# Performance work log

Hardware: AMD Instinct MI355X
Metric: run time of the kernel (lower is better)

Reference implementation:

```python
import jax, jax.numpy as jnp
import numpy as np

L = 2000          # number of residues (sequence length)
FEATURES_L = 2048 # config.features_L pad target
W = 7             # config.window_size
D = 54            # per-residue feature dim after bert_lin
H = 3             # attention heads
HD = D // H       # head dim = 18
CH = 32           # conv hidden channels
KS = (3, 5, 7)    # config.kernels


def setup_inputs() -> dict:
    key = jax.random.key(0)
    ks = jax.random.split(key, 20)
    n = lambda k, s, sc=0.02: jax.random.normal(k, s, jnp.float32) * sc
    return {
        'beft_f': jax.random.normal(ks[0], (L, 1024), jnp.float32),
        'pssm_f': jax.random.normal(ks[1], (L, 20), jnp.float32),
        'hmm_f': jax.random.normal(ks[2], (L, 30), jnp.float32),
        'dssp_f': jax.random.normal(ks[3], (L, 14), jnp.float32),
        'W_bert': n(ks[4], (1024, D)), 'b_bert': jnp.zeros((D,), jnp.float32),
        'ln_g1': jnp.ones((D,), jnp.float32), 'ln_b1': jnp.zeros((D,), jnp.float32),
        'ln_g2': jnp.ones((D,), jnp.float32), 'ln_b2': jnp.zeros((D,), jnp.float32),
        'conv1_w': n(ks[5], (CH, 1, 3, 1), 0.1), 'conv1_b': n(ks[6], (CH,), 0.1),
        'prelu_a': jnp.array(0.25, jnp.float32),
        'conv2_w': n(ks[7], (CH, 1, 5, 1), 0.1), 'conv2_b': n(ks[8], (CH,), 0.1),
        'conv3_w': n(ks[9], (CH, 1, 7, 1), 0.1), 'conv3_b': n(ks[10], (CH,), 0.1),
        'W1': n(ks[11], (972, 256)), 'b1': jnp.zeros((256,), jnp.float32),
        'W2': n(ks[12], (CH * 256, 256)), 'b2': jnp.zeros((256,), jnp.float32),
    }


def _ln(x, g, b, eps=1e-5):
    m = x.mean(-1, keepdims=True)
    v = ((x - m) ** 2).mean(-1, keepdims=True)
    return (x - m) * jax.lax.rsqrt(v + eps) * g + b


def _attn(x, g, b):
    # x: (L, W, D); no qkv projections, no 1/sqrt(d) scaling (as in source)
    qh = x.reshape(x.shape[0], W, H, HD)
    s = jnp.einsum('bqhd,bkhd->bhqk', qh, qh)
    p = jax.nn.softmax(s, axis=-1)
    o = jnp.einsum('bhqk,bkhd->bqhd', p, qh).reshape(x.shape[0], W, D)
    return _ln(o, g, b)


def _conv_branch(x, w, bias, k, act):
    pad = (k - 1) // 2
    c = jax.lax.conv_general_dilated(x, w, (1, 1), ((pad, pad), (0, 0)),
                                     dimension_numbers=('NCHW', 'OIHW', 'NCHW'))
    c = act(c + bias[None, :, None, None])
    c = jax.lax.reduce_window(c, -jnp.inf, jax.lax.max,
                              (1, 1, k, 1), (1, 1, 1, 1), 'VALID')
    return c.reshape(c.shape[0], CH, -1)  # (FEATURES_L, 32, (W-k+1)*2D)


def _forward(beft_f, W_bert, b_bert, ln_g1, ln_b1, ln_g2, ln_b2,
             conv1_w, conv1_b, prelu_a, conv2_w, conv2_b, conv3_w, conv3_b,
             W1, b1, W2, b2):
    f = beft_f @ W_bert + b_bert  # (L, 54)
    # sliding-window gather replicating the source python loop exactly:
    # interior rows i in (W, L-W): window = f[i-4 : i+3]; boundary rows: [f[i], 0...0]
    i = jnp.arange(L)
    j = jnp.arange(W)
    gidx = jnp.clip(i[:, None] - (W // 2 + 1) + j[None, :], 0, L - 1)
    win_int = f[gidx]                                   # (L, 7, 54)
    win_bnd = jnp.zeros((L, W, D), f.dtype).at[:, 0].set(f)
    boundary = (i <= W) | (i + W >= L)
    new_f = jnp.where(boundary[:, None, None], win_bnd, win_int)
    sf = _attn(new_f, ln_g1, ln_b1)
    sf = _attn(sf, ln_g2, ln_b2)
    cat = jnp.concatenate([new_f, sf], axis=2)          # (L, 7, 108)
    x = jnp.pad(cat, ((0, FEATURES_L - L), (0, 0), (0, 0)))[:, None]  # (FL,1,7,108)
    prelu = lambda z: jnp.where(z >= 0, z, prelu_a * z)
    feats = jnp.concatenate([
        _conv_branch(x, conv1_w, conv1_b, KS[0], prelu),
        _conv_branch(x, conv2_w, conv2_b, KS[1], jax.nn.relu),
        _conv_branch(x, conv3_w, conv3_b, KS[2], jax.nn.relu)], axis=2)  # (FL,32,972)
    y = feats[:L] @ W1 + b1                             # (L, 32, 256)
    y = y.reshape(L, CH * 256) @ W2 + b2                # (L, 256)
    return jnp.where(y >= 0, y, 0.01 * y)               # leaky_relu


def reference(beft_f, pssm_f, hmm_f, dssp_f, W_bert, b_bert, ln_g1, ln_b1,
              ln_g2, ln_b2, conv1_w, conv1_b, prelu_a, conv2_w, conv2_b,
              conv3_w, conv3_b, W1, b1, W2, b2):
    # pssm_f / hmm_f / dssp_f are accepted but unused in the source forward
    return _forward(beft_f, W_bert, b_bert, ln_g1, ln_b1, ln_g2, ln_b2,
                    conv1_w, conv1_b, prelu_a, conv2_w, conv2_b,
                    conv3_w, conv3_b, W1, b1, W2, b2)
```

## Files before the change

kernel.cpp:

```cpp
#include <hip/hip_runtime.h>

#define L_RES 2000
#define DF 54
#define WIN 7

typedef short bf16x8 __attribute__((ext_vector_type(8)));
typedef float f32x4 __attribute__((ext_vector_type(4)));
typedef unsigned short ushort8v __attribute__((ext_vector_type(8)));

__device__ __forceinline__ unsigned short f2bf(float f) {
    unsigned int u = __float_as_uint(f);
    unsigned int r = (u + 0x7FFFu + ((u >> 16) & 1u)) >> 16;
    return (unsigned short)r;
}
__device__ __forceinline__ float bf2f(unsigned short h) {
    return __uint_as_float(((unsigned int)h) << 16);
}
__device__ __forceinline__ void gload16(const unsigned short* g, unsigned short* l) {
    __builtin_amdgcn_global_load_lds(
        (const __attribute__((address_space(1))) void*)g,
        (__attribute__((address_space(3))) void*)l, 16, 0, 0);
}

__global__ __launch_bounds__(256) void split_beft(const float* __restrict__ beft,
                                                  unsigned short* __restrict__ A2) {
    int l = blockIdx.x;
    int t = threadIdx.x;
    unsigned short* row = A2 + (size_t)l * 3072;
    for (int k = t; k < 1024; k += 256) {
        unsigned short hi = 0, lo = 0;
        if (l < L_RES) {
            float x = beft[(size_t)l * 1024 + k];
            hi = f2bf(x);
            lo = f2bf(x - bf2f(hi));
        }
        row[k] = hi;
        row[1024 + k] = lo;
        row[2048 + k] = hi;
    }
}

__global__ __launch_bounds__(256) void b2t_build(const float* __restrict__ Wb,
                                                 unsigned short* __restrict__ B2T) {
    int idx = blockIdx.x * 256 + threadIdx.x;
    int n = idx / 3072, col = idx % 3072;
    int seg = col >> 10, k = col & 1023;
    unsigned short r = 0;
    if (n < DF) {
        float v = Wb[(size_t)k * DF + n];
        unsigned short hi = f2bf(v);
        r = (seg < 2) ? hi : f2bf(v - bf2f(hi));
    }
    B2T[idx] = r;
}

__global__ __launch_bounds__(256) void bert_mfma(const unsigned short* __restrict__ A2,
                                                 const unsigned short* __restrict__ B2T,
                                                 float* __restrict__ bpart) {
    __shared__ unsigned short ldsA[128 * 64];
    __shared__ unsigned short ldsB[64 * 64];
    int t = threadIdx.x, w = t >> 6, lane = t & 63;
    int m0 = blockIdx.x * 128;
    int z = blockIdx.y;
    long koff = (long)z * 768;
    int wr = w >> 1, wc = w & 1;
    int arow = lane & 15, kgrp = lane >> 4;

    const unsigned short* aS[4]; const unsigned short* bS[2];
    int aD[4], bD[2];
    #pragma unroll
    for (int j = 0; j < 4; ++j) {
        int s = j * 256 + t, r = s >> 3, c = s & 7;
        aS[j] = A2 + koff + (size_t)(m0 + r) * 3072 + c * 8;
        aD[j] = r * 64 + ((c ^ (r & 7)) * 8);
    }
    #pragma unroll
    for (int j = 0; j < 2; ++j) {
        int s = j * 256 + t, r = s >> 3, c = s & 7;
        bS[j] = B2T + koff + (size_t)r * 3072 + c * 8;
        bD[j] = r * 64 + ((c ^ (r & 7)) * 8);
    }
    f32x4 acc[4][2];
    #pragma unroll
    for (int mi = 0; mi < 4; ++mi)
        #pragma unroll
        for (int ni = 0; ni < 2; ++ni) acc[mi][ni] = (f32x4)(0.f);

    ushort8v va[4], vb[2];
    #pragma unroll
    for (int j = 0; j < 4; ++j) va[j] = *(const ushort8v*)(aS[j]);
    #pragma unroll
    for (int j = 0; j < 2; ++j) vb[j] = *(const ushort8v*)(bS[j]);

    for (int ks = 0; ks < 12; ++ks) {
        __syncthreads();
        #pragma unroll
        for (int j = 0; j < 4; ++j) *(ushort8v*)&ldsA[aD[j]] = va[j];
        #pragma unroll
        for (int j = 0; j < 2; ++j) *(ushort8v*)&ldsB[bD[j]] = vb[j];
        __syncthreads();
        if (ks + 1 < 12) {
            #pragma unroll
            for (int j = 0; j < 4; ++j) va[j] = *(const ushort8v*)(aS[j] + (ks + 1) * 64);
            #pragma unroll
            for (int j = 0; j < 2; ++j) vb[j] = *(const ushort8v*)(bS[j] + (ks + 1) * 64);
        }
        #pragma unroll
        for (int kk = 0; kk < 2; ++kk) {
            int chunk = kk * 4 + kgrp;
            bf16x8 af[4], bfr[2];
            #pragma unroll
            for (int mi = 0; mi < 4; ++mi) {
                int rl = wr * 64 + mi * 16 + arow;
                af[mi] = *(const bf16x8*)&ldsA[rl * 64 + ((chunk ^ (rl & 7)) * 8)];
            }
            #pragma unroll
            for (int ni = 0; ni < 2; ++ni) {
                int rl = wc * 32 + ni * 16 + arow;
                bfr[ni] = *(const bf16x8*)&ldsB[rl * 64 + ((chunk ^ (rl & 7)) * 8)];
            }
            #pragma unroll
            for (int mi = 0; mi < 4; ++mi)
                #pragma unroll
                for (int ni = 0; ni < 2; ++ni)
                    acc[mi][ni] = __builtin_amdgcn_mfma_f32_16x16x32_bf16(af[mi], bfr[ni], acc[mi][ni], 0, 0, 0);
        }
    }
    #pragma unroll
    for (int ni = 0; ni < 2; ++ni) {
        int n = wc * 32 + ni * 16 + arow;
        #pragma unroll
        for (int mi = 0; mi < 4; ++mi)
            #pragma unroll
            for (int r = 0; r < 4; ++r) {
                int m = m0 + wr * 64 + mi * 16 + kgrp * 4 + r;
                bpart[((size_t)z * 2048 + m) * 64 + n] = acc[mi][ni][r];
            }
    }
}

__global__ __launch_bounds__(64) void bert_reduce(const float* __restrict__ bpart,
                                                  const float* __restrict__ bb,
                                                  float* __restrict__ f) {
    int l = blockIdx.x, n = threadIdx.x;
    if (n < DF) {
        float s = bb[n];
        #pragma unroll
        for (int z = 0; z < 4; ++z) s += bpart[((size_t)z * 2048 + l) * 64 + n];
        f[(size_t)l * DF + n] = s;
    }
}

__device__ __forceinline__ void attn_layer(const float (*in)[DF], float (*out)[DF],
                                           float (*s)[WIN][WIN],
                                           const float* __restrict__ g,
                                           const float* __restrict__ b,
                                           float* mm, float* vv, int t) {
    for (int idx = t; idx < 3 * WIN * WIN; idx += 64) {
        int h = idx / 49, r = idx % 49, q = r / WIN, k = r % WIN;
        float sum = 0.f;
        #pragma unroll
        for (int d = 0; d < 18; ++d) sum = fmaf(in[q][h * 18 + d], in[k][h * 18 + d], sum);
        s[h][q][k] = sum;
    }
    __syncthreads();
    for (int idx = t; idx < 3 * WIN; idx += 64) {
        int h = idx / WIN, q = idx % WIN;
        float mx = s[h][q][0];
        #pragma unroll
        for (int k = 1; k < WIN; ++k) mx = fmaxf(mx, s[h][q][k]);
        float e[WIN], sum = 0.f;
        #pragma unroll
        for (int k = 0; k < WIN; ++k) { e[k] = expf(s[h][q][k] - mx); sum += e[k]; }
        float inv = 1.f / sum;
        #pragma unroll
        for (int k = 0; k < WIN; ++k) s[h][q][k] = e[k] * inv;
    }
    __syncthreads();
    for (int idx = t; idx < WIN * DF; idx += 64) {
        int q = idx / DF, c = idx % DF, h = c / 18;
        float sum = 0.f;
        #pragma unroll
        for (int k = 0; k < WIN; ++k) sum = fmaf(s[h][q][k], in[k][c], sum);
        out[q][c] = sum;
    }
    __syncthreads();
    for (int q = t; q < WIN; q += 64) {
        float m = 0.f;
        for (int c = 0; c < DF; ++c) m += out[q][c];
        m *= (1.f / DF);
        float v = 0.f;
        for (int c = 0; c < DF; ++c) { float d0 = out[q][c] - m; v = fmaf(d0, d0, v); }
        v *= (1.f / DF);
        mm[q] = m; vv[q] = rsqrtf(v + 1e-5f);
    }
    __syncthreads();
    for (int idx = t; idx < WIN * DF; idx += 64) {
        int q = idx / DF, c = idx % DF;
        out[q][c] = (out[q][c] - mm[q]) * vv[q] * g[c] + b[c];
    }
    __syncthreads();
}

__global__ __launch_bounds__(64) void window_attn(const float* __restrict__ f,
                                                  const float* __restrict__ g1,
                                                  const float* __restrict__ b1,
                                                  const float* __restrict__ g2,
                                                  const float* __restrict__ b2,
                                                  float* __restrict__ cat) {
    int l = blockIdx.x;
    int t = threadIdx.x;
    __shared__ float w[WIN][DF], o1[WIN][DF], o2[WIN][DF];
    __shared__ float s[3][WIN][WIN];
    __shared__ float mm[WIN], vv[WIN];
    bool boundary = (l <= WIN) || (l + WIN >= L_RES);
    for (int idx = t; idx < WIN * DF; idx += 64) {
        int j = idx / DF, d = idx % DF;
        w[j][d] = boundary ? (j == 0 ? f[(size_t)l * DF + d] : 0.f)
                           : f[(size_t)(l - 4 + j) * DF + d];
    }
    __syncthreads();
    attn_layer(w, o1, s, g1, b1, mm, vv, t);
    attn_layer(o1, o2, s, g2, b2, mm, vv, t);
    for (int idx = t; idx < WIN * DF; idx += 64) {
        int j = idx / DF, d = idx % DF;
        cat[(size_t)l * 756 + j * 108 + d] = w[j][d];
        cat[(size_t)l * 756 + j * 108 + DF + d] = o2[j][d];
    }
}

__global__ __launch_bounds__(256) void transpose_to_bf16(const float* __restrict__ src,
                                                         unsigned short* __restrict__ dst,
                                                         int M, int N, int Mpad) {
    __shared__ float tile[32][33];
    int m0 = blockIdx.x * 32, n0 = blockIdx.y * 32;
    int c = threadIdx.x % 32, r0 = threadIdx.x / 32;
    #pragma unroll
    for (int rr = 0; rr < 4; ++rr) {
        int r = r0 + rr * 8, m = m0 + r;
        tile[r][c] = (m < M) ? src[(size_t)m * N + n0 + c] : 0.f;
    }
    __syncthreads();
    #pragma unroll
    for (int rr = 0; rr < 4; ++rr) {
        int r = r0 + rr * 8;
        dst[(size_t)(n0 + r) * Mpad + m0 + c] = f2bf(tile[c][r]);
    }
}

__global__ __launch_bounds__(256) void conv_pool(
        const float* __restrict__ cat,
        const float* __restrict__ c1w, const float* __restrict__ c1b,
        const float* __restrict__ pa_p,
        const float* __restrict__ c2w, const float* __restrict__ c2b,
        const float* __restrict__ c3w, const float* __restrict__ c3b,
        unsigned short* __restrict__ Ap, int lbase) {
    int bid = blockIdx.x;
    int b = bid >> 2;
    int ch0 = (bid & 3) * 8;
    int l0 = lbase + b * 4;
    int t = threadIdx.x;
    __shared__ float catl[4 * 756];
    for (int i = t; i < 3024; i += 256) catl[i] = cat[(size_t)l0 * 756 + i];
    __syncthreads();
    float pa = pa_p[0];
    unsigned short* base = Ap + (size_t)b * 128 * 1024;
    int res = t >> 6, dp = t & 63;
    if (dp < 54) {
        int d0 = dp * 2;
        const float* cr = catl + res * 756;
        float colA[WIN], colB[WIN];
        #pragma unroll
        for (int h = 0; h < WIN; ++h) {
            colA[h] = cr[h * 108 + d0];
            colB[h] = cr[h * 108 + d0 + 1];
        }
        for (int c = ch0; c < ch0 + 8; ++c) {
            unsigned short* Arow = base + (size_t)(res * 32 + c) * 1024;
            {
                float w0 = c1w[c * 3], w1 = c1w[c * 3 + 1], w2 = c1w[c * 3 + 2];
                float bb = c1b[c];
                float vA[WIN], vB[WIN];
                #pragma unroll
                for (int h = 0; h < WIN; ++h) {
                    float sA = bb, sB = bb;
                    if (h >= 1) { sA = fmaf(w0, colA[h - 1], sA); sB = fmaf(w0, colB[h - 1], sB); }
                    sA = fmaf(w1, colA[h], sA); sB = fmaf(w1, colB[h], sB);
                    if (h <= 5) { sA = fmaf(w2, colA[h + 1], sA); sB = fmaf(w2, colB[h + 1], sB); }
                    vA[h] = sA >= 0.f ? sA : pa * sA;
                    vB[h] = sB >= 0.f ? sB : pa * sB;
                }
                #pragma unroll
                for (int p = 0; p < 5; ++p) {
                    unsigned int ua = f2bf(fmaxf(fmaxf(vA[p], vA[p + 1]), vA[p + 2]));
                    unsigned int ub = f2bf(fmaxf(fmaxf(vB[p], vB[p + 1]), vB[p + 2]));
                    *(unsigned int*)&Arow[p * 108 + d0] = ua | (ub << 16);
                }
            }
            {
                float wg[5], bb = c2b[c];
                #pragma unroll
                for (int x = 0; x < 5; ++x) wg[x] = c2w[c * 5 + x];
                float vA[WIN], vB[WIN];
                #pragma unroll
                for (int h = 0; h < WIN; ++h) {
                    float sA = bb, sB = bb;
                    #pragma unroll
                    for (int x = 0; x < 5; ++x) {
                        int hh = h + x - 2;
                        if (hh >= 0 && hh <= 6) {
                            sA = fmaf(wg[x], colA[hh], sA);
                            sB = fmaf(wg[x], colB[hh], sB);
                        }
                    }
                    vA[h] = fmaxf(sA, 0.f);
                    vB[h] = fmaxf(sB, 0.f);
                }
                #pragma unroll
                for (int p = 0; p < 3; ++p) {
                    float ma = vA[p], mb = vB[p];
                    #pragma unroll
                    for (int r = 1; r < 5; ++r) { ma = fmaxf(ma, vA[p + r]); mb = fmaxf(mb, vB[p + r]); }
                    unsigned int ua = f2bf(ma), ub = f2bf(mb);
                    *(unsigned int*)&Arow[540 + p * 108 + d0] = ua | (ub << 16);
                }
            }
            {
                float wg[7], bb = c3b[c];
                #pragma unroll
                for (int x = 0; x < 7; ++x) wg[x] = c3w[c * 7 + x];
                float ma = 0.f, mb = 0.f;
                #pragma unroll
                for (int h = 0; h < WIN; ++h) {
                    float sA = bb, sB = bb;
                    #pragma unroll
                    for (int x = 0; x < 7; ++x) {
                        int hh = h + x - 3;
                        if (hh >= 0 && hh <= 6) {
                            sA = fmaf(wg[x], colA[hh], sA);
                            sB = fmaf(wg[x], colB[hh], sB);
                        }
                    }
                    ma = fmaxf(ma, sA);
                    mb = fmaxf(mb, sB);
                }
                unsigned int ua = f2bf(fmaxf(ma, 0.f)), ub = f2bf(fmaxf(mb, 0.f));
                *(unsigned int*)&Arow[864 + d0] = ua | (ub << 16);
            }
        }
    }
    for (int i = t; i < 832; i += 256) {
        int r = i / 26, q = i - r * 26;
        int res2 = r >> 3, c2 = ch0 + (r & 7);
        *(unsigned int*)&base[(size_t)(res2 * 32 + c2) * 1024 + 972 + q * 2] = 0u;
    }
}

template<bool EPI_BF16, int ZBITS>
__global__ __launch_bounds__(512) void gemm_tile8(
        const unsigned short* __restrict__ A, long lda,
        const unsigned short* __restrict__ B, long ldb,
        int nk, const float* __restrict__ bias,
        unsigned short* __restrict__ outB, float* __restrict__ outF,
        long outRowBase) {
    __shared__ unsigned short ldsA[128 * 64];
    __shared__ unsigned short ldsB[256 * 64];
    int t = threadIdx.x, w = t >> 6, lane = t & 63;
    int bid = blockIdx.x;
    int z = bid & ((1 << ZBITS) - 1);
    long m0 = (long)(bid >> ZBITS) * 128;
    long koff = (long)z * (long)nk * 64;
    A += koff; B += koff;
    int wr = w >> 2, wc = w & 3;
    int arow = lane & 15, kgrp = lane >> 4;
    int ra = lane >> 3, cc = lane & 7;
    int csw = (cc ^ ra) * 8;

    const unsigned short* gA[2]; const unsigned short* gB[4];
    unsigned short* dA[2]; unsigned short* dB[4];
    #pragma unroll
    for (int j = 0; j < 2; ++j) {
        int rbase = j * 64 + w * 8;
        gA[j] = A + (size_t)(m0 + rbase + ra) * lda + csw;
        dA[j] = &ldsA[rbase * 64];
    }
    #pragma unroll
    for (int j = 0; j < 4; ++j) {
        int rbase = j * 64 + w * 8;
        gB[j] = B + (size_t)(rbase + ra) * ldb + csw;
        dB[j] = &ldsB[rbase * 64];
    }
    f32x4 acc[4][4];
    #pragma unroll
    for (int mi = 0; mi < 4; ++mi)
        #pragma unroll
        for (int ni = 0; ni < 4; ++ni) acc[mi][ni] = (f32x4)(0.f);

    for (int ks = 0; ks < nk; ++ks) {
        #pragma unroll
        for (int j = 0; j < 2; ++j) gload16(gA[j] + ks * 64, dA[j]);
        #pragma unroll
        for (int j = 0; j < 4; ++j) gload16(gB[j] + ks * 64, dB[j]);
        __syncthreads();
        #pragma unroll
        for (int kk = 0; kk < 2; ++kk) {
            int chunk = kk * 4 + kgrp;
            bf16x8 af[4], bfr[4];
            #pragma unroll
            for (int mi = 0; mi < 4; ++mi) {
                int rl = wr * 64 + mi * 16 + arow;
                af[mi] = *(const bf16x8*)&ldsA[rl * 64 + ((chunk ^ (rl & 7)) * 8)];
            }
            #pragma unroll
            for (int ni = 0; ni < 4; ++ni) {
                int rl = wc * 64 + ni * 16 + arow;
                bfr[ni] = *(const bf16x8*)&ldsB[rl * 64 + ((chunk ^ (rl & 7)) * 8)];
            }
            #pragma unroll
            for (int mi = 0; mi < 4; ++mi)
                #pragma unroll
                for (int ni = 0; ni < 4; ++ni)
                    acc[mi][ni] = __builtin_amdgcn_mfma_f32_16x16x32_bf16(af[mi], bfr[ni], acc[mi][ni], 0, 0, 0);
        }
        __syncthreads();
    }
    #pragma unroll
    for (int ni = 0; ni < 4; ++ni) {
        int n = wc * 64 + ni * 16 + arow;
        float bv = EPI_BF16 ? bias[n] : 0.f;
        #pragma unroll
        for (int mi = 0; mi < 4; ++mi)
            #pragma unroll
            for (int r = 0; r < 4; ++r) {
                long m = m0 + wr * 64 + mi * 16 + kgrp * 4 + r;
                if (EPI_BF16)
                    outB[(outRowBase + m) * 256 + n] = f2bf(acc[mi][ni][r] + bv);
                else
                    outF[((long)z * 2048 + m) * 256 + n] = acc[mi][ni][r];
            }
    }
}

__global__ __launch_bounds__(256) void reduce2(const float* __restrict__ part,
                                               const float* __restrict__ b2v,
                                               float* __restrict__ out) {
    int l = blockIdx.x, n = threadIdx.x;
    float sum = b2v[n];
    #pragma unroll
    for (int s = 0; s < 16; ++s) sum += part[((size_t)s * 2048 + l) * 256 + n];
    out[(size_t)l * 256 + n] = sum >= 0.f ? sum : 0.01f * sum;
}

extern "C" void kernel_launch(void* const* d_in, const int* in_sizes, int n_in,
                              void* d_out, int out_size, void* d_ws, size_t ws_size,
                              hipStream_t stream) {
    const float* beft = (const float*)d_in[0];
    const float* Wb  = (const float*)d_in[4];
    const float* bb  = (const float*)d_in[5];
    const float* g1  = (const float*)d_in[6];
    const float* b1  = (const float*)d_in[7];
    const float* g2  = (const float*)d_in[8];
    const float* b2  = (const float*)d_in[9];
    const float* c1w = (const float*)d_in[10];
    const float* c1b = (const float*)d_in[11];
    const float* pa  = (const float*)d_in[12];
    const float* c2w = (const float*)d_in[13];
    const float* c2b = (const float*)d_in[14];
    const float* c3w = (const float*)d_in[15];
    const float* c3b = (const float*)d_in[16];
    const float* W1  = (const float*)d_in[17];
    const float* b1v = (const float*)d_in[18];
    const float* W2  = (const float*)d_in[19];
    const float* b2v = (const float*)d_in[20];
    float* out = (float*)d_out;
    char* ws = (char*)d_ws;

    float*          f    = (float*)(ws + 0);
    float*          cat  = (float*)(ws + 524288);
    unsigned short* W1T  = (unsigned short*)(ws + 8388608);
    unsigned short* W2T  = (unsigned short*)(ws + 8912896);
    unsigned short* y1   = (unsigned short*)(ws + 13107200);
    unsigned short* A2   = (unsigned short*)(ws + 13107200);
    unsigned short* B2T  = (unsigned short*)(ws + 25690112);
    float*          bpart= (float*)(ws + 46661632);
    unsigned short* Ap   = (unsigned short*)(ws + 46661632);
    float*          part = (float*)(ws + 46661632);

    long avail = (long)ws_size - 46661632L;
    long tpc = avail / (128L * 1024L * 2L);
    if (tpc < 1) tpc = 1;
    if (tpc > 500) tpc = 500;

    split_beft<<<2048, 256, 0, stream>>>(beft, A2);
    b2t_build<<<768, 256, 0, stream>>>(Wb, B2T);
    bert_mfma<<<dim3(16, 4), 256, 0, stream>>>(A2, B2T, bpart);
    bert_reduce<<<L_RES, 64, 0, stream>>>(bpart, bb, f);
    window_attn<<<L_RES, 64, 0, stream>>>(f, g1, b1, g2, b2, cat);
    transpose_to_bf16<<<dim3(32, 8), 256, 0, stream>>>(W1, W1T, 972, 256, 1024);
    transpose_to_bf16<<<dim3(256, 8), 256, 0, stream>>>(W2, W2T, 8192, 256, 8192);

    for (long t0 = 0; t0 < 500; t0 += tpc) {
        long nt = (500 - t0 < tpc) ? (500 - t0) : tpc;
        conv_pool<<<(int)(nt * 4), 256, 0, stream>>>(cat, c1w, c1b, pa, c2w, c2b,
                                                     c3w, c3b, Ap, (int)(t0 * 4));
        gemm_tile8<true, 0><<<(int)nt, 512, 0, stream>>>(
            Ap, 1024, W1T, 1024, 16, b1v, y1, nullptr, t0 * 128);
    }
    gemm_tile8<false, 4><<<256, 512, 0, stream>>>(
        y1, 8192, W2T, 8192, 8, nullptr, nullptr, part, 0);
    reduce2<<<L_RES, 256, 0, stream>>>(part, b2v, out);
}
```

Before: 152.5 us.

## Pre-pack W1 into MFMA fragment layout and use dedicated first-stage GEMM

Adds a kernel that packs W1 into bf16 in the exact per-lane MFMA B-fragment order, so the first GEMM can load B operands straight from global memory into registers with no LDS staging. A new 256-thread GEMM kernel double-buffers only the A tile in LDS with an XOR swizzle, reads B fragments directly, and fuses the bias and bf16 store. This is meant to cut LDS traffic and synchronization in the W1 GEMM. The cost is that B is re-read from global or L2 by every block and each thread holds more accumulator registers.

```diff
diff --git a/kernel.cpp b/kernel.cpp
--- a/kernel.cpp
+++ b/kernel.cpp
@@ -248,6 +248,16 @@
     }
 }
 
+__global__ __launch_bounds__(256) void w1tp_build(const float* __restrict__ W1,
+                                                  unsigned short* __restrict__ P) {
+    int idx = blockIdx.x * 256 + threadIdx.x;
+    int e = idx & 7, l = (idx >> 3) & 63, g = (idx >> 9) & 31, nb = idx >> 14;
+    int ks = g >> 1, kk = g & 1;
+    int n = nb * 16 + (l & 15);
+    int k = ks * 64 + kk * 32 + (l >> 4) * 8 + e;
+    P[idx] = (k < 972) ? f2bf(W1[(size_t)k * 256 + n]) : (unsigned short)0;
+}
+
 __global__ __launch_bounds__(256) void conv_pool(
         const float* __restrict__ cat,
         const float* __restrict__ c1w, const float* __restrict__ c1b,
@@ -353,6 +363,78 @@
         int r = i / 26, q = i - r * 26;
         int res2 = r >> 3, c2 = ch0 + (r & 7);
         *(unsigned int*)&base[(size_t)(res2 * 32 + c2) * 1024 + 972 + q * 2] = 0u;
+    }
+}
+
+__global__ __launch_bounds__(256, 2) void gemm1k(
+        const unsigned short* __restrict__ A,
+        const unsigned short* __restrict__ P,
+        const float* __restrict__ b1v,
+        unsigned short* __restrict__ y1, long outRowBase) {
+    __shared__ unsigned short ldsA[2][128 * 64];
+    int t = threadIdx.x, w = t >> 6, lane = t & 63;
+    long m0 = (long)blockIdx.x * 128;
+    int arow = lane & 15, kgrp = lane >> 4;
+    int ra = lane >> 3, cc = lane & 7;
+    int csw = (cc ^ ra) * 8;
+
+    const unsigned short* gA[4]; int rb[4];
+    #pragma unroll
+    for (int j = 0; j < 4; ++j) {
+        int rbase = j * 32 + w * 8;
+        gA[j] = A + (size_t)(m0 + rbase + ra) * 1024 + csw;
+        rb[j] = rbase * 64;
+    }
+    f32x4 acc[8][4];
+    #pragma unroll
+    for (int mi = 0; mi < 8; ++mi)
+        #pragma unroll
+        for (int ni = 0; ni < 4; ++ni) acc[mi][ni] = (f32x4)(0.f);
+
+    #pragma unroll
+    for (int j = 0; j < 4; ++j) gload16(gA[j], &ldsA[0][rb[j]]);
+    __syncthreads();
+
+    for (int ks = 0; ks < 16; ++ks) {
+        int cur = ks & 1;
+        bf16x8 bfr[2][4];
+        #pragma unroll
+        for (int kk = 0; kk < 2; ++kk)
+            #pragma unroll
+            for (int ni = 0; ni < 4; ++ni)
+                bfr[kk][ni] = *(const bf16x8*)&P[(((size_t)(w * 4 + ni) * 32 + ks * 2 + kk) * 64 + lane) * 8];
+        if (ks + 1 < 16) {
+            #pragma unroll
+            for (int j = 0; j < 4; ++j) gload16(gA[j] + (ks + 1) * 64, &ldsA[cur ^ 1][rb[j]]);
+        }
+        #pragma unroll
+        for (int kk = 0; kk < 2; ++kk) {
+            int chunk = kk * 4 + kgrp;
+            bf16x8 af[8];
+            #pragma unroll
+            for (int mi = 0; mi < 8; ++mi) {
+                int rl = mi * 16 + arow;
+                af[mi] = *(const bf16x8*)&ldsA[cur][rl * 64 + ((chunk ^ (rl & 7)) * 8)];
+            }
+            #pragma unroll
+            for (int mi = 0; mi < 8; ++mi)
+                #pragma unroll
+                for (int ni = 0; ni < 4; ++ni)
+                    acc[mi][ni] = __builtin_amdgcn_mfma_f32_16x16x32_bf16(af[mi], bfr[kk][ni], acc[mi][ni], 0, 0, 0);
+        }
+        __syncthreads();
+    }
+    #pragma unroll
+    for (int ni = 0; ni < 4; ++ni) {
+        int n = w * 64 + ni * 16 + arow;
+        float bv = b1v[n];
+        #pragma unroll
+        for (int mi = 0; mi < 8; ++mi)
+            #pragma unroll
+            for (int r = 0; r < 4; ++r) {
+                long row = m0 + mi * 16 + kgrp * 4 + r;
+                y1[(outRowBase + row) * 256 + n] = f2bf(acc[mi][ni][r] + bv);
+            }
     }
 }
 
@@ -477,7 +559,7 @@
 
     float*          f    = (float*)(ws + 0);
     float*          cat  = (float*)(ws + 524288);
-    unsigned short* W1T  = (unsigned short*)(ws + 8388608);
+    unsigned short* W1Tp = (unsigned short*)(ws + 8388608);
     unsigned short* W2T  = (unsigned short*)(ws + 8912896);
     unsigned short* y1   = (unsigned short*)(ws + 13107200);
     unsigned short* A2   = (unsigned short*)(ws + 13107200);
@@ -496,15 +578,14 @@
     bert_mfma<<<dim3(16, 4), 256, 0, stream>>>(A2, B2T, bpart);
     bert_reduce<<<L_RES, 64, 0, stream>>>(bpart, bb, f);
     window_attn<<<L_RES, 64, 0, stream>>>(f, g1, b1, g2, b2, cat);
-    transpose_to_bf16<<<dim3(32, 8), 256, 0, stream>>>(W1, W1T, 972, 256, 1024);
+    w1tp_build<<<1024, 256, 0, stream>>>(W1, W1Tp);
     transpose_to_bf16<<<dim3(256, 8), 256, 0, stream>>>(W2, W2T, 8192, 256, 8192);
 
     for (long t0 = 0; t0 < 500; t0 += tpc) {
         long nt = (500 - t0 < tpc) ? (500 - t0) : tpc;
         conv_pool<<<(int)(nt * 4), 256, 0, stream>>>(cat, c1w, c1b, pa, c2w, c2b,
                                                      c3w, c3b, Ap, (int)(t0 * 4));
-        gemm_tile8<true, 0><<<(int)nt, 512, 0, stream>>>(
-            Ap, 1024, W1T, 1024, 16, b1v, y1, nullptr, t0 * 128);
+        gemm1k<<<(int)nt, 256, 0, stream>>>(Ap, W1Tp, b1v, y1, t0 * 128);
     }
     gemm_tile8<false, 4><<<256, 512, 0, stream>>>(
         y1, 8192, W2T, 8192, 8, nullptr, nullptr, part, 0);
```

Measured after the change: 145.6 us (median of 3 runs). -4.6%, faster.
